# Performance work log

Hardware: AMD Instinct MI355X
Metric: run time of the kernel (lower is better)

The kernel has to match this reference:

```python
import jax, jax.numpy as jnp
import numpy as np

jax.config.update("jax_enable_x64", True)  # I-BERT's FixedPointMul runs in double precision

# I-BERT IntSoftmax constants
COEF0 = 0.35815147
COEF1 = 0.96963238 / COEF0
COEF2 = 1.0 / COEF0
X0 = -0.6931          # -ln(2)
N_EXP = 30            # large integer n in int_exp
MAX_BIT = 32
OUTPUT_BIT = 8
ACT_BIT = 16

B, H, S = 1, 12, 2048


def sg(x):
    return jax.lax.stop_gradient(x)


def ste_round(x):
    # straight-through round (matches torch round_ste / SymmetricQuantFunction backward)
    return x + sg(jnp.round(x) - x)


def ste_floor(x):
    return x + sg(jnp.floor(x) - x)


def sym_scale(x_min, x_max, bits):
    # symmetric_linear_quantization_params: scale = clamp(max(|min|,|max|),1e-8)/(2^(b-1)-1)
    n = 2 ** (bits - 1) - 1
    s = jnp.maximum(jnp.abs(x_min), jnp.abs(x_max))
    return sg(jnp.maximum(s, 1e-8) / n)


def fixedpoint_mul(pre_act, pre_sf, z_sf, bits):
    # I-BERT fixedpoint_mul: requantize pre_act (granularity pre_sf) to scale z_sf
    # using a 31-bit mantissa frexp decomposition, computed in float64.
    n = 2 ** (bits - 1) - 1
    z_int = ste_round(pre_act.astype(jnp.float64) / pre_sf.astype(jnp.float64))
    new_scale = sg((pre_sf / z_sf).astype(jnp.float64))
    e = jnp.floor(jnp.log2(jnp.abs(new_scale))) + 1.0   # frexp exponent
    m_int = jnp.round((new_scale / 2.0 ** e) * 2.0 ** 31)  # 31-bit mantissa
    out = ste_round(z_int * m_int / 2.0 ** (31.0 - e))
    return jnp.clip(out, -n - 1, n).astype(jnp.float32)


def quant_softmax(x):
    n16 = 2 ** (ACT_BIT - 1) - 1
    # ---- outer QuantAct(16, symmetric), specified min/max = data min/max ----
    sf = sym_scale(sg(x.min()), sg(x.max()), ACT_BIT)
    x_int = jnp.clip(ste_round(x / sf), -n16 - 1, n16)
    quant_x = x_int * sf  # dequantized activation returned by QuantAct
    # ---- IntSoftmax ----
    xi = quant_x / sf
    xi = xi - xi.max(axis=-1, keepdims=True)
    # int_exp: shift-based exponential, exp(x) = 2^(-q) * exp(r), r in (-ln2, 0]
    x0_int = sg(jnp.floor(X0 / sf))               # negative integer
    xi = jnp.maximum(xi, N_EXP * x0_int)
    q = ste_floor(xi / x0_int)
    r = xi - x0_int * q
    # int_polynomial: 2nd-order poly approximation of exp on (-ln2, 0]
    b_int = sg(jnp.floor(COEF1 / sf))
    c_int = sg(jnp.floor(COEF2 / sf ** 2))
    z = r * (r + b_int) + c_int
    exp_sf = sg(COEF0 * sf ** 2) / 2.0 ** N_EXP
    exp_int = jnp.maximum(ste_floor(z * 2.0 ** (N_EXP - q)), 0.0)
    # ---- inner QuantAct(16): requantize exp to 16 bits to avoid overflow ----
    act_sf = sym_scale(sg(exp_int.min()), sg(exp_int.max()), ACT_BIT)
    exp_int16 = fixedpoint_mul(exp_int, exp_sf, act_sf, ACT_BIT)
    # ---- integer normalization to output_bit fixed point ----
    s = exp_int16.sum(axis=-1, keepdims=True)
    factor = ste_floor(2.0 ** MAX_BIT / s)
    out_int = ste_floor(exp_int16 * factor / 2.0 ** (MAX_BIT - OUTPUT_BIT))
    out_sf = 1.0 / 2.0 ** OUTPUT_BIT
    return out_int * out_sf  # softmax probs quantized to 1/256 grid


def setup_inputs() -> dict:
    key = jax.random.key(0)
    x = jax.random.normal(key, (B, H, S, S), dtype=jnp.float32)
    return {"x": x}


def reference(x):
    return quant_softmax(x)
```

## Files before the change

kernel.cpp:

```cpp
#include <hip/hip_runtime.h>
#include <math.h>


#define ROW_S 2048
#define MM_BLOCKS 1024

struct Scalars {
    double exp_sf_d;
    double m_int;
    double inv_pow;
    float  sf;
    float  x0_int;
    float  b_int;
    float  c_int;
    float  thirty_x0;
    float  _pad[3];
};

__global__ __launch_bounds__(256) void k_minmax(const float* __restrict__ x,
                                                float* __restrict__ pmin,
                                                float* __restrict__ pmax,
                                                int n4) {
    __shared__ float smin[256], smax[256];
    const int tid = threadIdx.x;
    float vmin = INFINITY, vmax = -INFINITY;
    const float4* x4 = (const float4*)x;
    for (int i = blockIdx.x * 256 + tid; i < n4; i += MM_BLOCKS * 256) {
        float4 v = x4[i];
        vmin = fminf(vmin, fminf(fminf(v.x, v.y), fminf(v.z, v.w)));
        vmax = fmaxf(vmax, fmaxf(fmaxf(v.x, v.y), fmaxf(v.z, v.w)));
    }
    smin[tid] = vmin; smax[tid] = vmax;
    __syncthreads();
    for (int o = 128; o > 0; o >>= 1) {
        if (tid < o) {
            smin[tid] = fminf(smin[tid], smin[tid + o]);
            smax[tid] = fmaxf(smax[tid], smax[tid + o]);
        }
        __syncthreads();
    }
    if (tid == 0) { pmin[blockIdx.x] = smin[0]; pmax[blockIdx.x] = smax[0]; }
}

__global__ __launch_bounds__(256) void k_scalars(const float* __restrict__ pmin,
                                                 const float* __restrict__ pmax,
                                                 Scalars* __restrict__ sc) {
    __shared__ float smin[256], smax[256];
    const int tid = threadIdx.x;
    float vmin = INFINITY, vmax = -INFINITY;
    for (int i = tid; i < MM_BLOCKS; i += 256) {
        vmin = fminf(vmin, pmin[i]);
        vmax = fmaxf(vmax, pmax[i]);
    }
    smin[tid] = vmin; smax[tid] = vmax;
    __syncthreads();
    for (int o = 128; o > 0; o >>= 1) {
        if (tid < o) {
            smin[tid] = fminf(smin[tid], smin[tid + o]);
            smax[tid] = fmaxf(smax[tid], smax[tid + o]);
        }
        __syncthreads();
    }
    if (tid == 0) {
        const float xmin = smin[0], xmax = smax[0];
        const float sabs  = fmaxf(fabsf(xmin), fabsf(xmax));
        const float sf    = __fdiv_rn(fmaxf(sabs, 1e-8f), 32767.0f);
        const float x0i   = floorf(__fdiv_rn((float)(-0.6931), sf));
        const float sfsq  = __fmul_rn(sf, sf);
        const float b_int = floorf(__fdiv_rn((float)(0.96963238 / 0.35815147), sf));
        const float c_int = floorf(__fdiv_rn((float)(1.0 / 0.35815147), sfsq));
        const float exp_sf = __fdiv_rn(__fmul_rn((float)(0.35815147), sfsq), 1073741824.0f);
        const float emax   = __fmul_rn(c_int, 1073741824.0f);
        const float act_sf = __fdiv_rn(fmaxf(emax, 1e-8f), 32767.0f);
        const float  nsf = __fdiv_rn(exp_sf, act_sf);
        const double ns  = (double)nsf;
        int E;
        (void)frexp(ns, &E);
        const double m_int = rint(ldexp(ns, 31 - E));
        sc->exp_sf_d  = (double)exp_sf;
        sc->m_int     = m_int;
        sc->inv_pow   = ldexp(1.0, E - 31);
        sc->sf        = sf;
        sc->x0_int    = x0i;
        sc->b_int     = b_int;
        sc->c_int     = c_int;
        sc->thirty_x0 = __fmul_rn(30.0f, x0i);
    }
}

__global__ __launch_bounds__(256) void k_row(const float* __restrict__ x,
                                             float* __restrict__ out,
                                             const Scalars* __restrict__ scp) {
    const int tid = threadIdx.x;
    const size_t rowbase = (size_t)blockIdx.x * ROW_S;
    const float4* x4 = (const float4*)(x + rowbase);
    float4* o4 = (float4*)(out + rowbase);

    const Scalars sc = *scp;
    const float sf = sc.sf;

    const float4 va = x4[tid];
    const float4 vb = x4[tid + 256];
    float xv[8] = {va.x, va.y, va.z, va.w, vb.x, vb.y, vb.z, vb.w};

    float xi[8];
    float vmax = -INFINITY;
#pragma unroll
    for (int j = 0; j < 8; ++j) {
        float t = rintf(__fdiv_rn(xv[j], sf));
        t = fminf(fmaxf(t, -32768.0f), 32767.0f);
        t = __fmul_rn(t, sf);
        t = __fdiv_rn(t, sf);
        xi[j] = t;
        vmax = fmaxf(vmax, t);
    }

    __shared__ float red[256];
    red[tid] = vmax;
    __syncthreads();
    for (int o = 128; o > 0; o >>= 1) {
        if (tid < o) red[tid] = fmaxf(red[tid], red[tid + o]);
        __syncthreads();
    }
    const float ximax = red[0];
    __syncthreads();

    float e16[8];
    float ssum = 0.0f;
#pragma unroll
    for (int j = 0; j < 8; ++j) {
        const float xs = __fsub_rn(xi[j], ximax);
        const float xm = fmaxf(xs, sc.thirty_x0);
        const float qf = floorf(__fdiv_rn(xm, sc.x0_int));
        const float r  = __fsub_rn(xm, __fmul_rn(sc.x0_int, qf));
        const float z  = __fadd_rn(__fmul_rn(r, __fadd_rn(r, sc.b_int)), sc.c_int);
        const int   qi = (int)qf;
        const float p2 = __int_as_float((157 - qi) << 23);
        const float ei = fmaxf(floorf(__fmul_rn(z, p2)), 0.0f);
        const double zi = rint((double)ei / sc.exp_sf_d);
        double ov = rint(__dmul_rn(zi, sc.m_int) * sc.inv_pow);
        ov = fmin(fmax(ov, -32768.0), 32767.0);
        const float v = (float)ov;
        e16[j] = v;
        ssum += v;
    }

    red[tid] = ssum;
    __syncthreads();
    for (int o = 128; o > 0; o >>= 1) {
        if (tid < o) red[tid] = red[tid] + red[tid + o];
        __syncthreads();
    }
    const float s = red[0];
    const float factor = floorf(__fdiv_rn(4294967296.0f, s));

    float ov[8];
#pragma unroll
    for (int j = 0; j < 8; ++j) {
        const float oi = floorf(__fdiv_rn(__fmul_rn(e16[j], factor), 16777216.0f));
        ov[j] = __fmul_rn(oi, 0.00390625f);
    }
    o4[tid]       = make_float4(ov[0], ov[1], ov[2], ov[3]);
    o4[tid + 256] = make_float4(ov[4], ov[5], ov[6], ov[7]);
}

extern "C" void kernel_launch(void* const* d_in, const int* in_sizes, int n_in,
                              void* d_out, int out_size, void* d_ws, size_t ws_size,
                              hipStream_t stream) {
    const float* x = (const float*)d_in[0];
    float* out = (float*)d_out;
    const int n = in_sizes[0];
    const int rows = n / ROW_S;

    Scalars* sc = (Scalars*)d_ws;
    float* pmin = (float*)((char*)d_ws + 64);
    float* pmax = pmin + MM_BLOCKS;

    k_minmax<<<MM_BLOCKS, 256, 0, stream>>>(x, pmin, pmax, n / 4);
    k_scalars<<<1, 256, 0, stream>>>(pmin, pmax, sc);
    k_row<<<rows, 256, 0, stream>>>(x, out, sc);
}
```

Before: 399.6 us.

## Replace divisions with reciprocal FMA, use wave shuffles, nontemporal stores

Replaces the IEEE float and double divisions in the row kernel with a multiply by a precomputed reciprocal plus one FMA correction step. The scalar kernel now stores those reciprocals alongside the other constants. All three kernels swap the shared-memory tree reductions for wave-level shuffle reductions, which cuts barriers. The minmax grid is doubled and the output is written with nontemporal stores. The corrected-reciprocal division may differ from true rounding in rare edge cases.

```diff
diff --git a/kernel.cpp b/kernel.cpp
--- a/kernel.cpp
+++ b/kernel.cpp
@@ -3,25 +3,40 @@
 
 
 #define ROW_S 2048
-#define MM_BLOCKS 1024
+#define MM_BLOCKS 2048
+
+typedef float floatx4 __attribute__((ext_vector_type(4)));
 
 struct Scalars {
     double exp_sf_d;
+    double inv_exp_sf;
     double m_int;
     double inv_pow;
     float  sf;
+    float  inv_sf;
     float  x0_int;
+    float  inv_x0;
     float  b_int;
     float  c_int;
     float  thirty_x0;
-    float  _pad[3];
+    float  _pad;
 };
+
+__device__ __forceinline__ float div_rn(float a, float b, float inv) {
+    const float q0 = __fmul_rn(a, inv);
+    const float r  = __fmaf_rn(-b, q0, a);
+    return __fmaf_rn(r, inv, q0);
+}
+__device__ __forceinline__ double ddiv_rn(double a, double b, double inv) {
+    const double q0 = __dmul_rn(a, inv);
+    const double r  = __fma_rn(-b, q0, a);
+    return __fma_rn(r, inv, q0);
+}
 
 __global__ __launch_bounds__(256) void k_minmax(const float* __restrict__ x,
                                                 float* __restrict__ pmin,
                                                 float* __restrict__ pmax,
                                                 int n4) {
-    __shared__ float smin[256], smax[256];
     const int tid = threadIdx.x;
     float vmin = INFINITY, vmax = -INFINITY;
     const float4* x4 = (const float4*)x;
@@ -30,39 +45,42 @@
         vmin = fminf(vmin, fminf(fminf(v.x, v.y), fminf(v.z, v.w)));
         vmax = fmaxf(vmax, fmaxf(fmaxf(v.x, v.y), fmaxf(v.z, v.w)));
     }
-    smin[tid] = vmin; smax[tid] = vmax;
-    __syncthreads();
-    for (int o = 128; o > 0; o >>= 1) {
-        if (tid < o) {
-            smin[tid] = fminf(smin[tid], smin[tid + o]);
-            smax[tid] = fmaxf(smax[tid], smax[tid + o]);
-        }
-        __syncthreads();
-    }
-    if (tid == 0) { pmin[blockIdx.x] = smin[0]; pmax[blockIdx.x] = smax[0]; }
+#pragma unroll
+    for (int m = 32; m > 0; m >>= 1) {
+        vmin = fminf(vmin, __shfl_xor(vmin, m));
+        vmax = fmaxf(vmax, __shfl_xor(vmax, m));
+    }
+    __shared__ float smin[4], smax[4];
+    const int wave = tid >> 6, lane = tid & 63;
+    if (lane == 0) { smin[wave] = vmin; smax[wave] = vmax; }
+    __syncthreads();
+    if (tid == 0) {
+        pmin[blockIdx.x] = fminf(fminf(smin[0], smin[1]), fminf(smin[2], smin[3]));
+        pmax[blockIdx.x] = fmaxf(fmaxf(smax[0], smax[1]), fmaxf(smax[2], smax[3]));
+    }
 }
 
 __global__ __launch_bounds__(256) void k_scalars(const float* __restrict__ pmin,
                                                  const float* __restrict__ pmax,
                                                  Scalars* __restrict__ sc) {
-    __shared__ float smin[256], smax[256];
     const int tid = threadIdx.x;
     float vmin = INFINITY, vmax = -INFINITY;
     for (int i = tid; i < MM_BLOCKS; i += 256) {
         vmin = fminf(vmin, pmin[i]);
         vmax = fmaxf(vmax, pmax[i]);
     }
-    smin[tid] = vmin; smax[tid] = vmax;
-    __syncthreads();
-    for (int o = 128; o > 0; o >>= 1) {
-        if (tid < o) {
-            smin[tid] = fminf(smin[tid], smin[tid + o]);
-            smax[tid] = fmaxf(smax[tid], smax[tid + o]);
-        }
-        __syncthreads();
-    }
+#pragma unroll
+    for (int m = 32; m > 0; m >>= 1) {
+        vmin = fminf(vmin, __shfl_xor(vmin, m));
+        vmax = fmaxf(vmax, __shfl_xor(vmax, m));
+    }
+    __shared__ float smin[4], smax[4];
+    const int wave = tid >> 6, lane = tid & 63;
+    if (lane == 0) { smin[wave] = vmin; smax[wave] = vmax; }
+    __syncthreads();
     if (tid == 0) {
-        const float xmin = smin[0], xmax = smax[0];
+        const float xmin = fminf(fminf(smin[0], smin[1]), fminf(smin[2], smin[3]));
+        const float xmax = fmaxf(fmaxf(smax[0], smax[1]), fmaxf(smax[2], smax[3]));
         const float sabs  = fmaxf(fabsf(xmin), fabsf(xmax));
         const float sf    = __fdiv_rn(fmaxf(sabs, 1e-8f), 32767.0f);
         const float x0i   = floorf(__fdiv_rn((float)(-0.6931), sf));
@@ -77,14 +95,17 @@
         int E;
         (void)frexp(ns, &E);
         const double m_int = rint(ldexp(ns, 31 - E));
-        sc->exp_sf_d  = (double)exp_sf;
-        sc->m_int     = m_int;
-        sc->inv_pow   = ldexp(1.0, E - 31);
-        sc->sf        = sf;
-        sc->x0_int    = x0i;
-        sc->b_int     = b_int;
-        sc->c_int     = c_int;
-        sc->thirty_x0 = __fmul_rn(30.0f, x0i);
+        sc->exp_sf_d   = (double)exp_sf;
+        sc->inv_exp_sf = 1.0 / (double)exp_sf;
+        sc->m_int      = m_int;
+        sc->inv_pow    = ldexp(1.0, E - 31);
+        sc->sf         = sf;
+        sc->inv_sf     = __fdiv_rn(1.0f, sf);
+        sc->x0_int     = x0i;
+        sc->inv_x0     = __fdiv_rn(1.0f, x0i);
+        sc->b_int      = b_int;
+        sc->c_int      = c_int;
+        sc->thirty_x0  = __fmul_rn(30.0f, x0i);
     }
 }
 
@@ -94,36 +115,35 @@
     const int tid = threadIdx.x;
     const size_t rowbase = (size_t)blockIdx.x * ROW_S;
     const float4* x4 = (const float4*)(x + rowbase);
-    float4* o4 = (float4*)(out + rowbase);
-
-    const Scalars sc = *scp;
-    const float sf = sc.sf;
+    floatx4* o4 = (floatx4*)(out + rowbase);
 
     const float4 va = x4[tid];
     const float4 vb = x4[tid + 256];
+
+    const Scalars sc = *scp;
+    const float sf = sc.sf, inv_sf = sc.inv_sf;
+
     float xv[8] = {va.x, va.y, va.z, va.w, vb.x, vb.y, vb.z, vb.w};
 
     float xi[8];
     float vmax = -INFINITY;
 #pragma unroll
     for (int j = 0; j < 8; ++j) {
-        float t = rintf(__fdiv_rn(xv[j], sf));
+        float t = rintf(div_rn(xv[j], sf, inv_sf));
         t = fminf(fmaxf(t, -32768.0f), 32767.0f);
         t = __fmul_rn(t, sf);
-        t = __fdiv_rn(t, sf);
+        t = div_rn(t, sf, inv_sf);
         xi[j] = t;
         vmax = fmaxf(vmax, t);
     }
 
-    __shared__ float red[256];
-    red[tid] = vmax;
-    __syncthreads();
-    for (int o = 128; o > 0; o >>= 1) {
-        if (tid < o) red[tid] = fmaxf(red[tid], red[tid + o]);
-        __syncthreads();
-    }
-    const float ximax = red[0];
-    __syncthreads();
+    __shared__ float red[8];
+    const int wave = tid >> 6, lane = tid & 63;
+#pragma unroll
+    for (int m = 32; m > 0; m >>= 1) vmax = fmaxf(vmax, __shfl_xor(vmax, m));
+    if (lane == 0) red[wave] = vmax;
+    __syncthreads();
+    const float ximax = fmaxf(fmaxf(red[0], red[1]), fmaxf(red[2], red[3]));
 
     float e16[8];
     float ssum = 0.0f;
@@ -131,37 +151,38 @@
     for (int j = 0; j < 8; ++j) {
         const float xs = __fsub_rn(xi[j], ximax);
         const float xm = fmaxf(xs, sc.thirty_x0);
-        const float qf = floorf(__fdiv_rn(xm, sc.x0_int));
+        const float qf = floorf(div_rn(xm, sc.x0_int, sc.inv_x0));
         const float r  = __fsub_rn(xm, __fmul_rn(sc.x0_int, qf));
         const float z  = __fadd_rn(__fmul_rn(r, __fadd_rn(r, sc.b_int)), sc.c_int);
         const int   qi = (int)qf;
         const float p2 = __int_as_float((157 - qi) << 23);
         const float ei = fmaxf(floorf(__fmul_rn(z, p2)), 0.0f);
-        const double zi = rint((double)ei / sc.exp_sf_d);
-        double ov = rint(__dmul_rn(zi, sc.m_int) * sc.inv_pow);
+        const double a  = (double)ei;
+        const double zi = rint(ddiv_rn(a, sc.exp_sf_d, sc.inv_exp_sf));
+        double ov = rint(__dmul_rn(__dmul_rn(zi, sc.m_int), sc.inv_pow));
         ov = fmin(fmax(ov, -32768.0), 32767.0);
         const float v = (float)ov;
         e16[j] = v;
         ssum += v;
     }
 
-    red[tid] = ssum;
-    __syncthreads();
-    for (int o = 128; o > 0; o >>= 1) {
-        if (tid < o) red[tid] = red[tid] + red[tid + o];
-        __syncthreads();
-    }
-    const float s = red[0];
+#pragma unroll
+    for (int m = 32; m > 0; m >>= 1) ssum += __shfl_xor(ssum, m);
+    if (lane == 0) red[4 + wave] = ssum;
+    __syncthreads();
+    const float s = ((red[4] + red[5]) + (red[6] + red[7]));
     const float factor = floorf(__fdiv_rn(4294967296.0f, s));
 
     float ov[8];
 #pragma unroll
     for (int j = 0; j < 8; ++j) {
-        const float oi = floorf(__fdiv_rn(__fmul_rn(e16[j], factor), 16777216.0f));
+        const float oi = floorf(__fmul_rn(__fmul_rn(e16[j], factor), 5.9604644775390625e-8f));
         ov[j] = __fmul_rn(oi, 0.00390625f);
     }
-    o4[tid]       = make_float4(ov[0], ov[1], ov[2], ov[3]);
-    o4[tid + 256] = make_float4(ov[4], ov[5], ov[6], ov[7]);
+    floatx4 w0 = {ov[0], ov[1], ov[2], ov[3]};
+    floatx4 w1 = {ov[4], ov[5], ov[6], ov[7]};
+    __builtin_nontemporal_store(w0, &o4[tid]);
+    __builtin_nontemporal_store(w1, &o4[tid + 256]);
 }
 
 extern "C" void kernel_launch(void* const* d_in, const int* in_sizes, int n_in,
@@ -173,7 +194,7 @@
     const int rows = n / ROW_S;
 
     Scalars* sc = (Scalars*)d_ws;
-    float* pmin = (float*)((char*)d_ws + 64);
+    float* pmin = (float*)((char*)d_ws + 256);
     float* pmax = pmin + MM_BLOCKS;
 
     k_minmax<<<MM_BLOCKS, 256, 0, stream>>>(x, pmin, pmax, n / 4);
```

New measurement: 355.1 us. 11.1% less time.
